# Performance work log

Measured on AMD Instinct MI355X. Metric: run time of the kernel, lower is better.

Reference implementation:

```python
import jax, jax.numpy as jnp
import numpy as np

N_NODES = 50000
N_EDGES = 1600000
N_REL = 8
D_IN = 128
D_HID = 128
D_OUT = 64
N_POOL = 256


def setup_inputs() -> dict:
    key = jax.random.key(0)
    ks = jax.random.split(key, 10)
    x = jax.random.uniform(ks[0], (N_NODES, D_IN), dtype=jnp.float32)
    edge_index = jax.random.randint(ks[1], (2, N_EDGES), 0, N_NODES)
    edge_type = jax.random.randint(ks[2], (N_EDGES,), 0, N_REL)
    pool_indices = jax.random.randint(ks[3], (N_POOL,), 0, N_NODES)
    s1 = 1.0 / np.sqrt(D_IN)
    s2 = 1.0 / np.sqrt(D_HID)
    W1 = jax.random.normal(ks[4], (N_REL, D_IN, D_HID), dtype=jnp.float32) * s1
    root1 = jax.random.normal(ks[5], (D_IN, D_HID), dtype=jnp.float32) * s1
    b1 = jnp.zeros((D_HID,), jnp.float32)
    W2 = jax.random.normal(ks[6], (N_REL, D_HID, D_OUT), dtype=jnp.float32) * s2
    root2 = jax.random.normal(ks[7], (D_HID, D_OUT), dtype=jnp.float32) * s2
    b2 = jnp.zeros((D_OUT,), jnp.float32)
    return {"x": x, "edge_index": edge_index, "edge_type": edge_type,
            "pool_indices": pool_indices, "W1": W1, "root1": root1, "b1": b1,
            "W2": W2, "root2": root2, "b2": b2}


def rgcn_layer(h, edge_index, edge_type, W, root, b):
    # PyG RGCNConv: out = h @ root + sum_r mean_{j in N_r(i)} (h_j @ W_r) + b
    src, dst = edge_index[0], edge_index[1]
    n = h.shape[0]
    r = W.shape[0]
    hW = jnp.einsum('nd,rdh->rnh', h, W)          # (R, N, H)
    msg = hW[edge_type, src]                      # (E, H) gather per edge
    seg = edge_type * n + dst                     # per-(relation, dst) segment
    agg = jax.ops.segment_sum(msg, seg, num_segments=r * n)
    agg = agg.reshape(r, n, -1)
    cnt = jax.ops.segment_sum(jnp.ones(msg.shape[0], h.dtype), seg,
                              num_segments=r * n).reshape(r, n, 1)
    mean = agg / jnp.maximum(cnt, 1.0)            # per-relation mean
    return mean.sum(0) + h @ root + b


def reference(x, edge_index, edge_type, pool_indices, W1, root1, b1, W2, root2, b2):
    h = jax.nn.relu(rgcn_layer(x, edge_index, edge_type, W1, root1, b1))
    node_embeddings = rgcn_layer(h, edge_index, edge_type, W2, root2, b2)
    selected_embeddings = node_embeddings[pool_indices]       # (P, D_OUT)
    type_features = x[pool_indices, :3]                       # (P, 3)
    weights = jnp.array([4.0, 1.0, 2.0], dtype=x.dtype)
    entity_weights = type_features @ weights                  # (P,)
    sum_of_weights = jnp.sum(entity_weights) + 1e-9
    pooled = jnp.sum(selected_embeddings * entity_weights[:, None], axis=0,
                     keepdims=True) / sum_of_weights          # (1, D_OUT)
    return pooled
```

## Files before the change

kernel.cpp:

```cpp
#include <hip/hip_runtime.h>

#define N_NODES 50000
#define N_EDGES 1600000
#define N_REL   8
#define D_IN    128
#define D_HID   128
#define D_OUT   64
#define N_POOL  256

#define CAP_S   12288
#define NSEG    (N_REL * CAP_S)
#define BUCKET  32
#define BUCKET2 32
#define NCODE   (N_REL * N_POOL)

typedef short v8s __attribute__((ext_vector_type(8)));
typedef float v4f __attribute__((ext_vector_type(4)));

constexpr size_t OFF_FILLC  = 0;
constexpr size_t OFF_FILLC2 = OFF_FILLC + NSEG;
constexpr size_t ZERO_ELEMS = OFF_FILLC2 + NCODE;
constexpr size_t OFF_PBIT   = ZERO_ELEMS;
constexpr size_t OFF_SBIT   = OFF_PBIT + 2048;
constexpr size_t OFF_CTR    = OFF_SBIT + 2048;
constexpr size_t OFF_PID    = OFF_CTR + 8;
constexpr size_t OFF_SID    = OFF_PID + N_NODES;
constexpr size_t OFF_PNODES = OFF_SID + N_NODES;
constexpr size_t OFF_SNODES = OFF_PNODES + N_POOL;
constexpr size_t OFF_SRCSLOT= OFF_SNODES + CAP_S;
constexpr size_t OFF_ESLOT2 = OFF_SRCSLOT + (size_t)NSEG * BUCKET;
constexpr size_t OFF_AGG1B  = OFF_ESLOT2 + (size_t)NCODE * BUCKET2;
constexpr size_t OFF_XALL   = OFF_AGG1B + (size_t)NSEG * 64;
constexpr size_t OFF_WT     = OFF_XALL + (size_t)N_NODES * 64;
constexpr size_t OFF_H      = OFF_WT + (size_t)1152 * 128 / 2;
constexpr size_t OFF_EMB    = OFF_H + (size_t)CAP_S * D_HID;
constexpr size_t TOTAL_ELEMS= OFF_EMB + (size_t)N_POOL * D_OUT;

__device__ __forceinline__ void atomAddF(float* p, float v) { unsafeAtomicAdd(p, v); }

__device__ __forceinline__ unsigned short f2bf(float f) {
  union { float f; unsigned u; } v; v.f = f;
  unsigned r = v.u + 0x7FFFu + ((v.u >> 16) & 1u);
  return (unsigned short)(r >> 16);
}
__device__ __forceinline__ float bfLo(unsigned v) { return __uint_as_float(v << 16); }
__device__ __forceinline__ float bfHi(unsigned v) { return __uint_as_float(v & 0xFFFF0000u); }

__global__ __launch_bounds__(256) void k_init(
    const int* __restrict__ pool, const float* __restrict__ x,
    const float* __restrict__ W1, const float* __restrict__ root1,
    float* __restrict__ ws) {
  unsigned* pBit = (unsigned*)(ws + OFF_PBIT);
  unsigned* sBit = (unsigned*)(ws + OFF_SBIT);
  int*      ctr  = (int*)(ws + OFF_CTR);
  unsigned* xall = (unsigned*)(ws + OFF_XALL);
  unsigned short* Wt = (unsigned short*)(ws + OFF_WT);
  int tid = threadIdx.x, bid = blockIdx.x;
  int gtid = bid * 256 + tid, gthr = gridDim.x * 256;
  int wave = tid >> 6, lane = tid & 63;

  float4 z = {0.f, 0.f, 0.f, 0.f};
  for (int i = gtid; i < (int)(ZERO_ELEMS / 4); i += gthr) ((float4*)ws)[i] = z;

  if (bid == 0) {
    for (int i = tid; i < 2048; i += 256) { pBit[i] = 0u; sBit[i] = 0u; }
    if (tid < 8) ctr[tid] = 0;
    __syncthreads();
    int node = pool[tid];
    unsigned bit = 1u << (node & 31);
    atomicOr(&pBit[node >> 5], bit);
    atomicOr(&sBit[node >> 5], bit);
  }

  int gw = (bid - 1) * 4 + wave;
  if (bid >= 1 && gw < 288) {
    int kt = gw >> 3, nt = gw & 7;
    int k0 = kt * 32 + ((lane >> 4) << 3);
    int n = nt * 16 + (lane & 15);
    v8s frag;
#pragma unroll
    for (int j = 0; j < 8; j++) {
      int kg = k0 + j;
      float v = (kg < 1024) ? W1[(size_t)kg * D_HID + n]
                            : root1[(size_t)(kg - 1024) * D_HID + n];
      frag[j] = (short)f2bf(v);
    }
    ((v8s*)Wt)[gw * 64 + lane] = frag;
  }

  for (int i = gtid; i < N_NODES * 64; i += gthr) {
    float2 v = ((const float2*)x)[i];
    xall[i] = ((unsigned)f2bf(v.y) << 16) | f2bf(v.x);
  }
}

__global__ __launch_bounds__(256) void k_pass1(
    const int* __restrict__ EI, const unsigned* __restrict__ pBit, unsigned* sBit) {
  int idx = blockIdx.x * 256 + threadIdx.x;
  if (idx >= N_EDGES / 4) return;
  int4 d4 = ((const int4*)(EI + N_EDGES))[idx];
  int d[4] = {d4.x, d4.y, d4.z, d4.w};
#pragma unroll
  for (int i = 0; i < 4; i++) {
    int dst = d[i];
    if ((pBit[dst >> 5] >> (dst & 31)) & 1u) {
      int src = EI[idx * 4 + i];
      atomicOr(&sBit[src >> 5], 1u << (src & 31));
    }
  }
}

__global__ __launch_bounds__(256) void k_compactS(
    const unsigned* __restrict__ sBit, const unsigned* __restrict__ pBit,
    int* sId, int* sNodes, int* pId, int* pNodes, int* ctr) {
  __shared__ int wcnt[4];
  __shared__ int sbase;
  int tid = threadIdx.x, wave = tid >> 6, lane = tid & 63;
  int node = blockIdx.x * 256 + tid;
  bool sp = (node < N_NODES) && ((sBit[node >> 5] >> (node & 31)) & 1u);
  unsigned long long m = __ballot(sp);
  if (lane == 0) wcnt[wave] = __popcll(m);
  __syncthreads();
  if (tid == 0) {
    int tot = wcnt[0] + wcnt[1] + wcnt[2] + wcnt[3];
    sbase = tot ? atomicAdd(&ctr[1], tot) : 0;
  }
  __syncthreads();
  if (sp) {
    int off = sbase;
    for (int w2 = 0; w2 < wave; w2++) off += wcnt[w2];
    int id = off + __popcll(m & ((1ull << lane) - 1ull));
    if (id < CAP_S) { sId[node] = id + 1; sNodes[id] = node; }
    else sId[node] = 0;
  }
  bool pp = (node < N_NODES) && ((pBit[node >> 5] >> (node & 31)) & 1u);
  unsigned long long pm = __ballot(pp);
  if (pm) {
    int leader = __ffsll(pm) - 1;
    int base = 0;
    if (lane == leader) base = atomicAdd(&ctr[0], __popcll(pm));
    base = __shfl(base, leader);
    if (pp) {
      int id = base + __popcll(pm & ((1ull << lane) - 1ull));
      pId[node] = id + 1;
      pNodes[id] = node;
    }
  }
}

__global__ __launch_bounds__(256) void k_fill(
    const int* __restrict__ EI, const int* __restrict__ ET,
    const unsigned* __restrict__ sBit, const unsigned* __restrict__ pBit,
    const int* __restrict__ sId, const int* __restrict__ pId,
    int* __restrict__ fillCtr, int* __restrict__ srcSlot,
    int* __restrict__ fillCtr2, int* __restrict__ eslot2) {
  int idx = blockIdx.x * 256 + threadIdx.x;
  if (idx >= N_EDGES / 4) return;
  int4 d4 = ((const int4*)(EI + N_EDGES))[idx];
  int d[4] = {d4.x, d4.y, d4.z, d4.w};
  bool any = false;
#pragma unroll
  for (int i = 0; i < 4; i++)
    any |= ((sBit[d[i] >> 5] >> (d[i] & 31)) & 1u) != 0u;
  if (!any) return;
  int4 t4 = ((const int4*)ET)[idx];
  int4 s4 = ((const int4*)EI)[idx];
  int t[4] = {t4.x, t4.y, t4.z, t4.w};
  int s[4] = {s4.x, s4.y, s4.z, s4.w};
#pragma unroll
  for (int i = 0; i < 4; i++) {
    int dst = d[i];
    if ((sBit[dst >> 5] >> (dst & 31)) & 1u) {
      int sp = sId[dst];
      if (sp > 0) {
        int seg = ((sp - 1) << 3) + t[i];
        int slot = atomicAdd(&fillCtr[seg], 1);
        if (slot < BUCKET) srcSlot[seg * BUCKET + slot] = s[i];
      }
      if ((pBit[dst >> 5] >> (dst & 31)) & 1u) {
        int code = t[i] * N_POOL + (pId[dst] - 1);
        int sl = sId[s[i]] - 1;
        if (sl >= 0) {
          int slot = atomicAdd(&fillCtr2[code], 1);
          if (slot < BUCKET2) eslot2[code * BUCKET2 + slot] = sl;
        }
      }
    }
  }
}

__global__ __launch_bounds__(256) void k_gather(
    const int* __restrict__ fillCtr, const int* __restrict__ srcSlot,
    const unsigned* __restrict__ xall, const int* __restrict__ ctr,
    unsigned* __restrict__ agg1b) {
  int w = (blockIdx.x << 2) + (threadIdx.x >> 6);
  if (w >= (ctr[1] << 3)) return;
  int lane = threadIdx.x & 63;
  int cnt = fillCtr[w];
  if (cnt > BUCKET) cnt = BUCKET;
  const int* slot = srcSlot + w * BUCKET;
  float a0 = 0.f, a1 = 0.f;
  int i = 0;
  for (; i + 4 <= cnt; i += 4) {
    int s0 = slot[i + 0];
    int s1 = slot[i + 1];
    int s2 = slot[i + 2];
    int s3 = slot[i + 3];
    unsigned v0 = xall[(size_t)s0 * 64 + lane];
    unsigned v1 = xall[(size_t)s1 * 64 + lane];
    unsigned v2 = xall[(size_t)s2 * 64 + lane];
    unsigned v3 = xall[(size_t)s3 * 64 + lane];
    a0 += (bfLo(v0) + bfLo(v1)) + (bfLo(v2) + bfLo(v3));
    a1 += (bfHi(v0) + bfHi(v1)) + (bfHi(v2) + bfHi(v3));
  }
  for (; i < cnt; i++) {
    unsigned v = xall[(size_t)slot[i] * 64 + lane];
    a0 += bfLo(v);
    a1 += bfHi(v);
  }
  float inv = 1.0f / fmaxf((float)cnt, 1.0f);
  agg1b[(size_t)w * 64 + lane] = ((unsigned)f2bf(a1 * inv) << 16) | f2bf(a0 * inv);
}

__global__ __launch_bounds__(256) void k_gemm1(
    const unsigned short* __restrict__ agg1b, const unsigned short* __restrict__ xall,
    const unsigned short* __restrict__ Wt, const float* __restrict__ b1,
    const int* __restrict__ sNodes, const int* __restrict__ ctr,
    float* __restrict__ h) {
  __shared__ float red[4][16][64];
  int sCount = ctr[1];
  int s0 = blockIdx.x * 16;
  if (s0 >= sCount) return;
  int colTile = blockIdx.y;
  int wave = threadIdx.x >> 6, lane = threadIdx.x & 63;
  int quad = lane >> 4, mn = lane & 15;
  int srow = s0 + mn;
  int g = (srow < sCount) ? sNodes[srow] : 0;
  v4f acc[4];
#pragma unroll
  for (int i = 0; i < 4; i++) acc[i] = (v4f){0.f, 0.f, 0.f, 0.f};
  const v8s* WtF = (const v8s*)Wt;
  int kt0 = wave * 9, kt1 = kt0 + 9;
  for (int kt = kt0; kt < kt1; kt++) {
    const unsigned short* aptr;
    if (kt < 32) {
      int r = kt >> 2;
      int d0 = (kt & 3) * 32 + quad * 8;
      aptr = agg1b + ((size_t)((srow << 3) + r) * 128 + d0);
    } else {
      int d0 = (kt - 32) * 32 + quad * 8;
      aptr = xall + ((size_t)g * 128 + d0);
    }
    v8s afrag = *(const v8s*)aptr;
    const v8s* wrow = WtF + (size_t)(kt * 8 + colTile * 4) * 64 + lane;
#pragma unroll
    for (int nt = 0; nt < 4; nt++) {
      v8s bfrag = wrow[nt * 64];
      acc[nt] = __builtin_amdgcn_mfma_f32_16x16x32_bf16(afrag, bfrag, acc[nt], 0, 0, 0);
    }
  }
#pragma unroll
  for (int nt = 0; nt < 4; nt++)
#pragma unroll
    for (int reg = 0; reg < 4; reg++)
      red[wave][nt * 4 + reg][lane] = acc[nt][reg];
  __syncthreads();
  int nt2 = threadIdx.x >> 6;
  int lane2 = threadIdx.x & 63;
  int quad2 = lane2 >> 4, mn2 = lane2 & 15;
#pragma unroll
  for (int reg = 0; reg < 4; reg++) {
    int idx = nt2 * 4 + reg;
    float v = red[0][idx][lane2] + red[1][idx][lane2]
            + red[2][idx][lane2] + red[3][idx][lane2];
    int s = s0 + quad2 * 4 + reg;
    int col = colTile * 64 + nt2 * 16 + mn2;
    if (s < sCount)
      h[(size_t)s * D_HID + col] = fmaxf(v + b1[col], 0.0f);
  }
}

__global__ __launch_bounds__(256) void k_gemm2(
    const float* __restrict__ W2, const float* __restrict__ root2,
    const float* __restrict__ b2,
    const int* __restrict__ fillCtr2, const int* __restrict__ eslot2,
    const int* __restrict__ pNodes, const int* __restrict__ sId,
    const int* __restrict__ ctr, const float* __restrict__ h,
    float* __restrict__ emb) {
  __shared__ float a[N_REL * D_HID + D_HID];
  __shared__ float partial[256];
  int pl = blockIdx.x;
  if (pl >= ctr[0]) return;
  int tid = threadIdx.x, wave = tid >> 6, lane = tid & 63;
#pragma unroll
  for (int rr = 0; rr < 2; rr++) {
    int r = wave * 2 + rr;
    int code = r * N_POOL + pl;
    int cnt = fillCtr2[code]; if (cnt > BUCKET2) cnt = BUCKET2;
    const int* sl = eslot2 + code * BUCKET2;
    float s0 = 0.f, s1 = 0.f;
    for (int i = 0; i < cnt; i++) {
      float2 v = ((const float2*)h)[(size_t)sl[i] * 64 + lane];
      s0 += v.x; s1 += v.y;
    }
    float inv = 1.0f / fmaxf((float)cnt, 1.0f);
    a[r * 128 + lane * 2]     = s0 * inv;
    a[r * 128 + lane * 2 + 1] = s1 * inv;
  }
  if (tid < 128) {
    int slp = sId[pNodes[pl]] - 1;
    a[1024 + tid] = h[(size_t)slp * D_HID + tid];
  }
  __syncthreads();
  int lo = wave * 288, hi = lo + 288;
  float acc = 0.0f;
  int hiW = (hi < 1024) ? hi : 1024;
#pragma unroll 4
  for (int k = lo; k < hiW; k++) acc += a[k] * W2[(size_t)k * D_OUT + lane];
  int loR = (lo > 1024) ? lo : 1024;
#pragma unroll 4
  for (int k = loR; k < hi; k++) acc += a[k] * root2[(size_t)(k - 1024) * D_OUT + lane];
  partial[tid] = acc;
  __syncthreads();
  if (tid < 64) {
    float r4 = partial[tid] + partial[tid + 64] + partial[tid + 128] + partial[tid + 192];
    emb[(size_t)pl * D_OUT + tid] = r4 + b2[tid];
  }
}

__global__ __launch_bounds__(256) void k_pool(
    const float* __restrict__ x, const int* __restrict__ pool,
    const int* __restrict__ pId, const float* __restrict__ emb,
    float* __restrict__ out) {
  __shared__ float ew[N_POOL];
  __shared__ int pls[N_POOL];
  int tid = threadIdx.x;
  int node = pool[tid];
  const float* xr = x + (size_t)node * D_IN;
  ew[tid] = 4.0f * xr[0] + 1.0f * xr[1] + 2.0f * xr[2];
  pls[tid] = pId[node] - 1;
  __syncthreads();
  if (tid < D_OUT) {
    float sw = 0.0f;
    for (int j = 0; j < N_POOL; j++) sw += ew[j];
    float acc = 0.0f;
    for (int j = 0; j < N_POOL; j++) acc += ew[j] * emb[(size_t)pls[j] * D_OUT + tid];
    out[tid] = acc / (sw + 1e-9f);
  }
}

extern "C" void kernel_launch(void* const* d_in, const int* in_sizes, int n_in,
                              void* d_out, int out_size, void* d_ws, size_t ws_size,
                              hipStream_t stream) {
  const float* x     = (const float*)d_in[0];
  const int*   EI    = (const int*)  d_in[1];
  const int*   ET    = (const int*)  d_in[2];
  const int*   pool  = (const int*)  d_in[3];
  const float* W1    = (const float*)d_in[4];
  const float* root1 = (const float*)d_in[5];
  const float* b1    = (const float*)d_in[6];
  const float* W2    = (const float*)d_in[7];
  const float* root2 = (const float*)d_in[8];
  const float* b2    = (const float*)d_in[9];
  float* out = (float*)d_out;
  float* ws  = (float*)d_ws;

  int*      fillCtr = (int*)(ws + OFF_FILLC);
  int*      fillCtr2= (int*)(ws + OFF_FILLC2);
  unsigned* pBit    = (unsigned*)(ws + OFF_PBIT);
  unsigned* sBit    = (unsigned*)(ws + OFF_SBIT);
  int*      ctr     = (int*)(ws + OFF_CTR);
  int*      pId     = (int*)(ws + OFF_PID);
  int*      sId     = (int*)(ws + OFF_SID);
  int*      pNodes  = (int*)(ws + OFF_PNODES);
  int*      sNodes  = (int*)(ws + OFF_SNODES);
  int*      srcSlot = (int*)(ws + OFF_SRCSLOT);
  int*      eslot2  = (int*)(ws + OFF_ESLOT2);
  unsigned* agg1b   = (unsigned*)(ws + OFF_AGG1B);
  unsigned* xall    = (unsigned*)(ws + OFF_XALL);
  unsigned short* Wt = (unsigned short*)(ws + OFF_WT);
  float*    h       = ws + OFF_H;
  float*    emb     = ws + OFF_EMB;

  k_init<<<1024, 256, 0, stream>>>(pool, x, W1, root1, ws);
  k_pass1<<<(N_EDGES / 4 + 255) / 256, 256, 0, stream>>>(EI, pBit, sBit);
  k_compactS<<<(N_NODES + 255) / 256, 256, 0, stream>>>(sBit, pBit, sId, sNodes, pId, pNodes, ctr);
  k_fill<<<(N_EDGES / 4 + 255) / 256, 256, 0, stream>>>(
      EI, ET, sBit, pBit, sId, pId, fillCtr, srcSlot, fillCtr2, eslot2);
  k_gather<<<NSEG / 4, 256, 0, stream>>>(fillCtr, srcSlot, xall, ctr, agg1b);
  k_gemm1<<<dim3(CAP_S / 16, 2), 256, 0, stream>>>(
      (const unsigned short*)agg1b, (const unsigned short*)xall, Wt, b1, sNodes, ctr, h);
  k_gemm2<<<N_POOL, 256, 0, stream>>>(
      W2, root2, b2, fillCtr2, eslot2, pNodes, sId, ctr, h, emb);
  k_pool<<<1, 256, 0, stream>>>(x, pool, pId, emb, out);
}
```

Baseline: 212.5 us.

## Retile gather, gemm1, pool kernels and vectorize bf16 conversion

The x-to-bf16 conversion now reads float4 and writes 64-bit words. The gather kernel becomes grid-stride with a fixed 2048-block grid instead of one wave per segment slot. gemm1 drops the split-K plus shared-memory reduction: each wave owns two column tiles over the full K, so the block y-dimension and the __syncthreads go away. The pool reduction is spread over four waves, and gemm2 unroll factors are raised. Together these aim to cut launch and reduction overhead, at the cost of longer per-wave serial K loops in gemm1.

Result: faster. 188.0 us (-11.5%).

```diff
diff --git a/kernel.cpp b/kernel.cpp
--- a/kernel.cpp
+++ b/kernel.cpp
@@ -53,7 +53,7 @@
   unsigned* pBit = (unsigned*)(ws + OFF_PBIT);
   unsigned* sBit = (unsigned*)(ws + OFF_SBIT);
   int*      ctr  = (int*)(ws + OFF_CTR);
-  unsigned* xall = (unsigned*)(ws + OFF_XALL);
+  unsigned long long* xall8 = (unsigned long long*)(ws + OFF_XALL);
   unsigned short* Wt = (unsigned short*)(ws + OFF_WT);
   int tid = threadIdx.x, bid = blockIdx.x;
   int gtid = bid * 256 + tid, gthr = gridDim.x * 256;
@@ -88,9 +88,11 @@
     ((v8s*)Wt)[gw * 64 + lane] = frag;
   }
 
-  for (int i = gtid; i < N_NODES * 64; i += gthr) {
-    float2 v = ((const float2*)x)[i];
-    xall[i] = ((unsigned)f2bf(v.y) << 16) | f2bf(v.x);
+  for (int i = gtid; i < N_NODES * 32; i += gthr) {
+    float4 v = ((const float4*)x)[i];
+    unsigned lo = ((unsigned)f2bf(v.y) << 16) | f2bf(v.x);
+    unsigned hi = ((unsigned)f2bf(v.w) << 16) | f2bf(v.z);
+    xall8[i] = (unsigned long long)lo | ((unsigned long long)hi << 32);
   }
 }
 
@@ -193,33 +195,35 @@
     const int* __restrict__ fillCtr, const int* __restrict__ srcSlot,
     const unsigned* __restrict__ xall, const int* __restrict__ ctr,
     unsigned* __restrict__ agg1b) {
-  int w = (blockIdx.x << 2) + (threadIdx.x >> 6);
-  if (w >= (ctr[1] << 3)) return;
+  int total = ctr[1] << 3;
   int lane = threadIdx.x & 63;
-  int cnt = fillCtr[w];
-  if (cnt > BUCKET) cnt = BUCKET;
-  const int* slot = srcSlot + w * BUCKET;
-  float a0 = 0.f, a1 = 0.f;
-  int i = 0;
-  for (; i + 4 <= cnt; i += 4) {
-    int s0 = slot[i + 0];
-    int s1 = slot[i + 1];
-    int s2 = slot[i + 2];
-    int s3 = slot[i + 3];
-    unsigned v0 = xall[(size_t)s0 * 64 + lane];
-    unsigned v1 = xall[(size_t)s1 * 64 + lane];
-    unsigned v2 = xall[(size_t)s2 * 64 + lane];
-    unsigned v3 = xall[(size_t)s3 * 64 + lane];
-    a0 += (bfLo(v0) + bfLo(v1)) + (bfLo(v2) + bfLo(v3));
-    a1 += (bfHi(v0) + bfHi(v1)) + (bfHi(v2) + bfHi(v3));
-  }
-  for (; i < cnt; i++) {
-    unsigned v = xall[(size_t)slot[i] * 64 + lane];
-    a0 += bfLo(v);
-    a1 += bfHi(v);
-  }
-  float inv = 1.0f / fmaxf((float)cnt, 1.0f);
-  agg1b[(size_t)w * 64 + lane] = ((unsigned)f2bf(a1 * inv) << 16) | f2bf(a0 * inv);
+  int wstride = gridDim.x << 2;
+  for (int w = (blockIdx.x << 2) + (threadIdx.x >> 6); w < total; w += wstride) {
+    int cnt = fillCtr[w];
+    if (cnt > BUCKET) cnt = BUCKET;
+    const int* slot = srcSlot + w * BUCKET;
+    float a0 = 0.f, a1 = 0.f;
+    int i = 0;
+    for (; i + 4 <= cnt; i += 4) {
+      int s0 = slot[i + 0];
+      int s1 = slot[i + 1];
+      int s2 = slot[i + 2];
+      int s3 = slot[i + 3];
+      unsigned v0 = xall[(size_t)s0 * 64 + lane];
+      unsigned v1 = xall[(size_t)s1 * 64 + lane];
+      unsigned v2 = xall[(size_t)s2 * 64 + lane];
+      unsigned v3 = xall[(size_t)s3 * 64 + lane];
+      a0 += (bfLo(v0) + bfLo(v1)) + (bfLo(v2) + bfLo(v3));
+      a1 += (bfHi(v0) + bfHi(v1)) + (bfHi(v2) + bfHi(v3));
+    }
+    for (; i < cnt; i++) {
+      unsigned v = xall[(size_t)slot[i] * 64 + lane];
+      a0 += bfLo(v);
+      a1 += bfHi(v);
+    }
+    float inv = 1.0f / fmaxf((float)cnt, 1.0f);
+    agg1b[(size_t)w * 64 + lane] = ((unsigned)f2bf(a1 * inv) << 16) | f2bf(a0 * inv);
+  }
 }
 
 __global__ __launch_bounds__(256) void k_gemm1(
@@ -227,21 +231,18 @@
     const unsigned short* __restrict__ Wt, const float* __restrict__ b1,
     const int* __restrict__ sNodes, const int* __restrict__ ctr,
     float* __restrict__ h) {
-  __shared__ float red[4][16][64];
   int sCount = ctr[1];
   int s0 = blockIdx.x * 16;
   if (s0 >= sCount) return;
-  int colTile = blockIdx.y;
   int wave = threadIdx.x >> 6, lane = threadIdx.x & 63;
   int quad = lane >> 4, mn = lane & 15;
   int srow = s0 + mn;
   int g = (srow < sCount) ? sNodes[srow] : 0;
-  v4f acc[4];
-#pragma unroll
-  for (int i = 0; i < 4; i++) acc[i] = (v4f){0.f, 0.f, 0.f, 0.f};
+  v4f acc[2];
+  acc[0] = (v4f){0.f, 0.f, 0.f, 0.f};
+  acc[1] = (v4f){0.f, 0.f, 0.f, 0.f};
   const v8s* WtF = (const v8s*)Wt;
-  int kt0 = wave * 9, kt1 = kt0 + 9;
-  for (int kt = kt0; kt < kt1; kt++) {
+  for (int kt = 0; kt < 36; kt++) {
     const unsigned short* aptr;
     if (kt < 32) {
       int r = kt >> 2;
@@ -252,31 +253,20 @@
       aptr = xall + ((size_t)g * 128 + d0);
     }
     v8s afrag = *(const v8s*)aptr;
-    const v8s* wrow = WtF + (size_t)(kt * 8 + colTile * 4) * 64 + lane;
-#pragma unroll
-    for (int nt = 0; nt < 4; nt++) {
-      v8s bfrag = wrow[nt * 64];
-      acc[nt] = __builtin_amdgcn_mfma_f32_16x16x32_bf16(afrag, bfrag, acc[nt], 0, 0, 0);
-    }
-  }
-#pragma unroll
-  for (int nt = 0; nt < 4; nt++)
-#pragma unroll
-    for (int reg = 0; reg < 4; reg++)
-      red[wave][nt * 4 + reg][lane] = acc[nt][reg];
-  __syncthreads();
-  int nt2 = threadIdx.x >> 6;
-  int lane2 = threadIdx.x & 63;
-  int quad2 = lane2 >> 4, mn2 = lane2 & 15;
-#pragma unroll
-  for (int reg = 0; reg < 4; reg++) {
-    int idx = nt2 * 4 + reg;
-    float v = red[0][idx][lane2] + red[1][idx][lane2]
-            + red[2][idx][lane2] + red[3][idx][lane2];
-    int s = s0 + quad2 * 4 + reg;
-    int col = colTile * 64 + nt2 * 16 + mn2;
-    if (s < sCount)
-      h[(size_t)s * D_HID + col] = fmaxf(v + b1[col], 0.0f);
+    const v8s* wrow = WtF + (size_t)(kt * 8 + wave * 2) * 64 + lane;
+    acc[0] = __builtin_amdgcn_mfma_f32_16x16x32_bf16(afrag, wrow[0],  acc[0], 0, 0, 0);
+    acc[1] = __builtin_amdgcn_mfma_f32_16x16x32_bf16(afrag, wrow[64], acc[1], 0, 0, 0);
+  }
+#pragma unroll
+  for (int nt = 0; nt < 2; nt++) {
+    int col = (wave * 2 + nt) * 16 + mn;
+    float bias = b1[col];
+#pragma unroll
+    for (int reg = 0; reg < 4; reg++) {
+      int s = s0 + quad * 4 + reg;
+      if (s < sCount)
+        h[(size_t)s * D_HID + col] = fmaxf(acc[nt][reg] + bias, 0.0f);
+    }
   }
 }
 
@@ -315,10 +305,10 @@
   int lo = wave * 288, hi = lo + 288;
   float acc = 0.0f;
   int hiW = (hi < 1024) ? hi : 1024;
-#pragma unroll 4
+#pragma unroll 8
   for (int k = lo; k < hiW; k++) acc += a[k] * W2[(size_t)k * D_OUT + lane];
   int loR = (lo > 1024) ? lo : 1024;
-#pragma unroll 4
+#pragma unroll 8
   for (int k = loR; k < hi; k++) acc += a[k] * root2[(size_t)(k - 1024) * D_OUT + lane];
   partial[tid] = acc;
   __syncthreads();
@@ -334,18 +324,25 @@
     float* __restrict__ out) {
   __shared__ float ew[N_POOL];
   __shared__ int pls[N_POOL];
-  int tid = threadIdx.x;
+  __shared__ float part[4][64];
+  int tid = threadIdx.x, wave = tid >> 6, lane = tid & 63;
   int node = pool[tid];
   const float* xr = x + (size_t)node * D_IN;
   ew[tid] = 4.0f * xr[0] + 1.0f * xr[1] + 2.0f * xr[2];
   pls[tid] = pId[node] - 1;
   __syncthreads();
-  if (tid < D_OUT) {
+  float acc = 0.0f;
+  int j0 = wave * 64;
+#pragma unroll 8
+  for (int j = j0; j < j0 + 64; j++)
+    acc += ew[j] * emb[(size_t)pls[j] * D_OUT + lane];
+  part[wave][lane] = acc;
+  __syncthreads();
+  if (tid < 64) {
     float sw = 0.0f;
     for (int j = 0; j < N_POOL; j++) sw += ew[j];
-    float acc = 0.0f;
-    for (int j = 0; j < N_POOL; j++) acc += ew[j] * emb[(size_t)pls[j] * D_OUT + tid];
-    out[tid] = acc / (sw + 1e-9f);
+    float r4 = part[0][tid] + part[1][tid] + part[2][tid] + part[3][tid];
+    out[tid] = r4 / (sw + 1e-9f);
   }
 }
 
@@ -387,8 +384,8 @@
   k_compactS<<<(N_NODES + 255) / 256, 256, 0, stream>>>(sBit, pBit, sId, sNodes, pId, pNodes, ctr);
   k_fill<<<(N_EDGES / 4 + 255) / 256, 256, 0, stream>>>(
       EI, ET, sBit, pBit, sId, pId, fillCtr, srcSlot, fillCtr2, eslot2);
-  k_gather<<<NSEG / 4, 256, 0, stream>>>(fillCtr, srcSlot, xall, ctr, agg1b);
-  k_gemm1<<<dim3(CAP_S / 16, 2), 256, 0, stream>>>(
+  k_gather<<<2048, 256, 0, stream>>>(fillCtr, srcSlot, xall, ctr, agg1b);
+  k_gemm1<<<CAP_S / 16, 256, 0, stream>>>(
       (const unsigned short*)agg1b, (const unsigned short*)xall, Wt, b1, sNodes, ctr, h);
   k_gemm2<<<N_POOL, 256, 0, stream>>>(
       W2, root2, b2, fillCtr2, eslot2, pNodes, sId, ctr, h, emb);
```
